# Kernel optimization log

Hardware: AMD Instinct MI355X
Metric: run time of the kernel (lower is better)

Reference implementation:

```python
import jax, jax.numpy as jnp
import numpy as np

B, N, C, H = 64, 4096, 128, 4
ALPHA = 0.2  # leaky_relu negative slope


def setup_inputs() -> dict:
    key = jax.random.key(0)
    k1, k2, k3, k4, k5 = jax.random.split(key, 5)
    V = jax.random.normal(k1, (B, N, C), dtype=jnp.float32)
    graph_size = jax.random.randint(k2, (B,), 1, N + 1, dtype=jnp.int32)
    # xavier_uniform-like init for weight [C, H*C] and tune_weight [1, H, C]
    lim_w = float(np.sqrt(6.0 / (C + H * C)))
    weight = jax.random.uniform(k3, (C, H * C), minval=-lim_w, maxval=lim_w, dtype=jnp.float32)
    lim_t = float(np.sqrt(6.0 / (H + C)))
    tune_weight = jax.random.uniform(k4, (1, H, C), minval=-lim_t, maxval=lim_t, dtype=jnp.float32)
    bias = jnp.full((H * C,), 0.01, dtype=jnp.float32)
    return {"V": V, "graph_size": graph_size, "weight": weight, "bias": bias, "tune_weight": tune_weight}


def reference(V, graph_size, weight, bias, tune_weight):
    # valid-node mask: node n of graph b is valid iff n < graph_size[b]
    mask = jnp.arange(N)[None, :] < graph_size[:, None]          # [B, N]
    # linear projection: [B, N, C] @ [C, H*C] + bias -> [B, N, H, C]
    Vg = (jnp.einsum('bnc,cd->bnd', V, weight) + bias).reshape(B, N, H, C)
    # attention logits per head: sum over features of tune_weight * Vg
    a = jnp.einsum('bnhc,ohc->bnh', Vg, tune_weight)             # [B, N, H]
    a = jnp.where(a >= 0, a, ALPHA * a)                          # leaky_relu
    # per-graph (segment) softmax over valid nodes
    a = jnp.where(mask[:, :, None], a, -jnp.inf)
    a = jax.nn.softmax(a, axis=1)                                # [B, N, H]
    # weighted segment sum -> [B, H, C] -> [B, H*C] (concat=True)
    out = jnp.einsum('bnhc,bnh->bhc', Vg, a)
    return out.reshape(B, H * C)
```

## Files before the change

### kernel.cpp

```cpp
#include <hip/hip_runtime.h>

#define NB 64
#define NN 4096
#define NC 128
#define NH 4
#define HC (NH * NC)
#define PSTRIDE (8 + HC)
#define NSLICE 64
#define TROWS 64
#define LRELU 0.2f

__global__ __launch_bounds__(128) void k0_wt(const float* __restrict__ W,
                                             const float* __restrict__ bias,
                                             const float* __restrict__ tune,
                                             float* __restrict__ wtbt)
{
    const int bid = blockIdx.x;
    const int t = threadIdx.x;
    const float* src = (bid < NC) ? (W + (size_t)bid * HC) : bias;
    float* dst = (bid < NC) ? (wtbt + bid * NH) : (wtbt + NC * NH);
    const float4 a = reinterpret_cast<const float4*>(src)[t];
    const float4 b = reinterpret_cast<const float4*>(tune)[t];
    float p = a.x * b.x + a.y * b.y + a.z * b.z + a.w * b.w;
    #pragma unroll
    for (int off = 16; off; off >>= 1) p += __shfl_xor(p, off, 32);
    if ((t & 31) == 0) dst[t >> 5] = p;
}

__global__ __launch_bounds__(256, 4) void k1_part(const float* __restrict__ V,
                                                  const int* __restrict__ gs,
                                                  const float* __restrict__ wtbt,
                                                  float* __restrict__ part)
{
    __shared__ float smem[8192];
    float (*Vt)[NC] = reinterpret_cast<float(*)[NC]>(smem);
    float (*Sall)[NH][132] = reinterpret_cast<float(*)[NH][132]>(smem);
    float* llds = smem + 8 * NH * 132;

    const int slice = blockIdx.x;
    const int b = blockIdx.y;
    const int tid = threadIdx.x;
    const int hw = tid >> 5;
    const int lane = tid & 31;
    const int h = lane >> 3;
    const int j = lane & 7;
    const int gsz = gs[b];

    const int segB = (gsz + NSLICE - 1) / NSLICE;
    const int myBeg = slice * segB;
    int myEnd = myBeg + segB;
    if (myEnd > gsz) myEnd = gsz;
    const bool hasWork = (myEnd > myBeg);

    float l = 0.f;
    float S[16] = {};

    if (hasWork) {
        float wtk[16];
        #pragma unroll
        for (int u = 0; u < 16; ++u) wtk[u] = wtbt[(16 * j + u) * NH + h];
        const float bt = wtbt[HC + h];

        const float4* Vg4 = reinterpret_cast<const float4*>(V);
        const size_t gbase = (size_t)b * NN;

        float4 r[8];
        #pragma unroll
        for (int k = 0; k < 8; ++k) {
            const int idx = tid + (k << 8);
            const int gr = myBeg + (idx >> 5);
            const int src_row = (gr < myEnd) ? gr : myBeg;
            r[k] = Vg4[(gbase + src_row) * 32 + (idx & 31)];
        }
        #pragma unroll
        for (int k = 0; k < 8; ++k) {
            const int idx = tid + (k << 8);
            reinterpret_cast<float4*>(smem)[idx] = r[k];
        }
        __syncthreads();
        #pragma unroll 2
        for (int rr = 0; rr < 8; ++rr) {
            const int row = (hw << 3) + rr;
            const bool valid = (myBeg + row < myEnd);
            const float4* vr = reinterpret_cast<const float4*>(&Vt[row][j * 16]);
            const float4 A0 = vr[0];
            const float4 A1 = vr[1];
            const float4 A2 = vr[2];
            const float4 A3 = vr[3];
            float a0 = A0.x * wtk[0]  + A0.y * wtk[1]  + A0.z * wtk[2]  + A0.w * wtk[3];
            float a1 = A1.x * wtk[4]  + A1.y * wtk[5]  + A1.z * wtk[6]  + A1.w * wtk[7];
            float a2 = A2.x * wtk[8]  + A2.y * wtk[9]  + A2.z * wtk[10] + A2.w * wtk[11];
            float a3 = A3.x * wtk[12] + A3.y * wtk[13] + A3.z * wtk[14] + A3.w * wtk[15];
            float lg = (a0 + a1) + (a2 + a3);
            lg += __shfl_xor(lg, 1, 32);
            lg += __shfl_xor(lg, 2, 32);
            lg += __shfl_xor(lg, 4, 32);
            float x = lg + bt;
            x = (x >= 0.f) ? x : LRELU * x;
            float p = __expf(x);
            p = valid ? p : 0.f;
            l += p;
            S[0]  += p * A0.x;  S[1]  += p * A0.y;  S[2]  += p * A0.z;  S[3]  += p * A0.w;
            S[4]  += p * A1.x;  S[5]  += p * A1.y;  S[6]  += p * A1.z;  S[7]  += p * A1.w;
            S[8]  += p * A2.x;  S[9]  += p * A2.y;  S[10] += p * A2.z;  S[11] += p * A2.w;
            S[12] += p * A3.x;  S[13] += p * A3.y;  S[14] += p * A3.z;  S[15] += p * A3.w;
        }
        __syncthreads();
    }

    if (j == 0) llds[hw * NH + h] = l;
    #pragma unroll
    for (int t = 0; t < 4; ++t) {
        float4 s4;
        s4.x = S[4 * t]; s4.y = S[4 * t + 1]; s4.z = S[4 * t + 2]; s4.w = S[4 * t + 3];
        *reinterpret_cast<float4*>(&Sall[hw][h][16 * j + 4 * t]) = s4;
    }
    __syncthreads();
    float* pb = part + (size_t)(b * NSLICE + slice) * PSTRIDE;
    if (tid < 4) {
        float L = 0.f;
        #pragma unroll
        for (int ww = 0; ww < 8; ++ww) L += llds[ww * NH + tid];
        pb[4 + tid] = L;
    }
    #pragma unroll
    for (int r2 = 0; r2 < 2; ++r2) {
        const int e = tid + r2 * 256;
        const int hh = e >> 7, k = e & 127;
        float s = 0.f;
        #pragma unroll
        for (int ww = 0; ww < 8; ++ww) s += Sall[ww][hh][k];
        pb[8 + e] = s;
    }
}

__global__ __launch_bounds__(128) void k2_out(const float* __restrict__ part,
                                              const float* __restrict__ W,
                                              const float* __restrict__ bias,
                                              float* __restrict__ out)
{
    const int b = blockIdx.x;
    const int h = blockIdx.y;
    const int tid = threadIdx.x;
    const float* pb = part + (size_t)b * NSLICE * PSTRIDE;

    __shared__ float Sn[NC];
    __shared__ float sL;
    if (tid < 64) {
        float lv = pb[(size_t)tid * PSTRIDE + 4 + h];
        #pragma unroll
        for (int off = 32; off; off >>= 1) lv += __shfl_down(lv, off, 64);
        if (tid == 0) sL = lv;
    }
    __syncthreads();
    {
        float s = 0.f;
        #pragma unroll 8
        for (int c = 0; c < NSLICE; ++c)
            s += pb[(size_t)c * PSTRIDE + 8 + h * NC + tid];
        Sn[tid] = s / sL;
    }
    __syncthreads();
    const int d = h * NC + tid;
    float acc = 0.f;
    #pragma unroll 4
    for (int k = 0; k < NC; ++k) acc += Sn[k] * W[(size_t)k * HC + d];
    out[(size_t)b * HC + d] = acc + bias[d];
}

extern "C" void kernel_launch(void* const* d_in, const int* in_sizes, int n_in,
                              void* d_out, int out_size, void* d_ws, size_t ws_size,
                              hipStream_t stream)
{
    const float* V    = (const float*)d_in[0];
    const int*   gsz  = (const int*)d_in[1];
    const float* W    = (const float*)d_in[2];
    const float* bias = (const float*)d_in[3];
    const float* tune = (const float*)d_in[4];
    float* out  = (float*)d_out;
    float* wtbt = (float*)d_ws;
    float* part = wtbt + PSTRIDE;

    hipLaunchKernelGGL(k0_wt, dim3(NC + 1), dim3(128), 0, stream, W, bias, tune, wtbt);
    hipLaunchKernelGGL(k1_part, dim3(NSLICE, NB), dim3(256), 0, stream, V, gsz, wtbt, part);
    hipLaunchKernelGGL(k2_out, dim3(NB, NH), dim3(128), 0, stream, part, W, bias, out);
}
```

Before: 51.67 us.

## Schedule fixed 64-row tiles across a persistent grid via a precomputed tile table

Per-graph fixed slicing (64 slices per graph regardless of size) is replaced by 64-row tiles. A tile table and per-graph prefix offsets are built in the setup kernel. A persistent grid of 1024 blocks strides over only the tiles that exist, and the output kernel reduces a variable number of partials per graph. The aim is to cut wasted blocks, partially filled row slices and partial-sum traffic for small graphs. In exchange it adds a serial scan in the setup kernel and extra synchronisation per loop iteration.

Measured after the change: 47.30 us. 8.5% less time.

```diff
diff --git a/kernel.cpp b/kernel.cpp
--- a/kernel.cpp
+++ b/kernel.cpp
@@ -6,70 +6,94 @@
 #define NH 4
 #define HC (NH * NC)
 #define PSTRIDE (8 + HC)
-#define NSLICE 64
 #define TROWS 64
+#define NBLK 1024
+#define MAXT 4096
 #define LRELU 0.2f
+
+#define WS_STARTS 520
+#define WS_TABLE  585
+#define WS_PART   (WS_TABLE + MAXT)
 
 __global__ __launch_bounds__(128) void k0_wt(const float* __restrict__ W,
                                              const float* __restrict__ bias,
                                              const float* __restrict__ tune,
-                                             float* __restrict__ wtbt)
+                                             const int* __restrict__ gs,
+                                             float* __restrict__ ws)
 {
     const int bid = blockIdx.x;
     const int t = threadIdx.x;
-    const float* src = (bid < NC) ? (W + (size_t)bid * HC) : bias;
-    float* dst = (bid < NC) ? (wtbt + bid * NH) : (wtbt + NC * NH);
-    const float4 a = reinterpret_cast<const float4*>(src)[t];
-    const float4 b = reinterpret_cast<const float4*>(tune)[t];
-    float p = a.x * b.x + a.y * b.y + a.z * b.z + a.w * b.w;
-    #pragma unroll
-    for (int off = 16; off; off >>= 1) p += __shfl_xor(p, off, 32);
-    if ((t & 31) == 0) dst[t >> 5] = p;
+    if (bid <= NC) {
+        const float* src = (bid < NC) ? (W + (size_t)bid * HC) : bias;
+        float* dst = (bid < NC) ? (ws + bid * NH) : (ws + NC * NH);
+        const float4 a = reinterpret_cast<const float4*>(src)[t];
+        const float4 b = reinterpret_cast<const float4*>(tune)[t];
+        float p = a.x * b.x + a.y * b.y + a.z * b.z + a.w * b.w;
+        #pragma unroll
+        for (int off = 16; off; off >>= 1) p += __shfl_xor(p, off, 32);
+        if ((t & 31) == 0) dst[t >> 5] = p;
+    } else {
+        __shared__ int ntile[NB], st[NB + 1];
+        if (t < NB) ntile[t] = (gs[t] + TROWS - 1) / TROWS;
+        __syncthreads();
+        if (t == 0) {
+            int acc = 0;
+            for (int b2 = 0; b2 < NB; ++b2) { st[b2] = acc; acc += ntile[b2]; }
+            st[NB] = acc;
+        }
+        __syncthreads();
+        int* wsI = reinterpret_cast<int*>(ws);
+        if (t < NB + 1) wsI[WS_STARTS + t] = st[t];
+        if (t < NB) {
+            const int s0 = st[t], n0 = ntile[t];
+            for (int w = 0; w < n0; ++w) wsI[WS_TABLE + s0 + w] = (t << 16) | w;
+        }
+    }
 }
 
 __global__ __launch_bounds__(256, 4) void k1_part(const float* __restrict__ V,
                                                   const int* __restrict__ gs,
-                                                  const float* __restrict__ wtbt,
-                                                  float* __restrict__ part)
+                                                  float* __restrict__ ws)
 {
     __shared__ float smem[8192];
     float (*Vt)[NC] = reinterpret_cast<float(*)[NC]>(smem);
     float (*Sall)[NH][132] = reinterpret_cast<float(*)[NH][132]>(smem);
     float* llds = smem + 8 * NH * 132;
 
-    const int slice = blockIdx.x;
-    const int b = blockIdx.y;
+    const int* wsI = reinterpret_cast<const int*>(ws);
+    const int T = wsI[WS_STARTS + NB];
+    const int* tab = wsI + WS_TABLE;
+    float* part = ws + WS_PART;
+    const float* wtbt = ws;
+
     const int tid = threadIdx.x;
     const int hw = tid >> 5;
     const int lane = tid & 31;
     const int h = lane >> 3;
     const int j = lane & 7;
-    const int gsz = gs[b];
-
-    const int segB = (gsz + NSLICE - 1) / NSLICE;
-    const int myBeg = slice * segB;
-    int myEnd = myBeg + segB;
-    if (myEnd > gsz) myEnd = gsz;
-    const bool hasWork = (myEnd > myBeg);
-
-    float l = 0.f;
-    float S[16] = {};
-
-    if (hasWork) {
-        float wtk[16];
-        #pragma unroll
-        for (int u = 0; u < 16; ++u) wtk[u] = wtbt[(16 * j + u) * NH + h];
-        const float bt = wtbt[HC + h];
-
-        const float4* Vg4 = reinterpret_cast<const float4*>(V);
+
+    float wtk[16];
+    #pragma unroll
+    for (int u = 0; u < 16; ++u) wtk[u] = wtbt[(16 * j + u) * NH + h];
+    const float bt = wtbt[HC + h];
+
+    const float4* Vg4 = reinterpret_cast<const float4*>(V);
+
+    for (int jt = blockIdx.x; jt < T; jt += NBLK) {
+        const int ent = tab[jt];
+        const int b = ent >> 16;
+        const int tbase = (ent & 0xffff) * TROWS;
+        const int gsz = gs[b];
+        int tend = tbase + TROWS;
+        if (tend > gsz) tend = gsz;
         const size_t gbase = (size_t)b * NN;
 
         float4 r[8];
         #pragma unroll
         for (int k = 0; k < 8; ++k) {
             const int idx = tid + (k << 8);
-            const int gr = myBeg + (idx >> 5);
-            const int src_row = (gr < myEnd) ? gr : myBeg;
+            const int gr = tbase + (idx >> 5);
+            const int src_row = (gr < tend) ? gr : tbase;
             r[k] = Vg4[(gbase + src_row) * 32 + (idx & 31)];
         }
         #pragma unroll
@@ -78,10 +102,13 @@
             reinterpret_cast<float4*>(smem)[idx] = r[k];
         }
         __syncthreads();
+
+        float l = 0.f;
+        float S[16] = {};
         #pragma unroll 2
         for (int rr = 0; rr < 8; ++rr) {
             const int row = (hw << 3) + rr;
-            const bool valid = (myBeg + row < myEnd);
+            const bool valid = (tbase + row < tend);
             const float4* vr = reinterpret_cast<const float4*>(&Vt[row][j * 16]);
             const float4 A0 = vr[0];
             const float4 A1 = vr[1];
@@ -106,35 +133,36 @@
             S[12] += p * A3.x;  S[13] += p * A3.y;  S[14] += p * A3.z;  S[15] += p * A3.w;
         }
         __syncthreads();
-    }
-
-    if (j == 0) llds[hw * NH + h] = l;
-    #pragma unroll
-    for (int t = 0; t < 4; ++t) {
-        float4 s4;
-        s4.x = S[4 * t]; s4.y = S[4 * t + 1]; s4.z = S[4 * t + 2]; s4.w = S[4 * t + 3];
-        *reinterpret_cast<float4*>(&Sall[hw][h][16 * j + 4 * t]) = s4;
-    }
-    __syncthreads();
-    float* pb = part + (size_t)(b * NSLICE + slice) * PSTRIDE;
-    if (tid < 4) {
-        float L = 0.f;
-        #pragma unroll
-        for (int ww = 0; ww < 8; ++ww) L += llds[ww * NH + tid];
-        pb[4 + tid] = L;
-    }
-    #pragma unroll
-    for (int r2 = 0; r2 < 2; ++r2) {
-        const int e = tid + r2 * 256;
-        const int hh = e >> 7, k = e & 127;
-        float s = 0.f;
-        #pragma unroll
-        for (int ww = 0; ww < 8; ++ww) s += Sall[ww][hh][k];
-        pb[8 + e] = s;
-    }
-}
-
-__global__ __launch_bounds__(128) void k2_out(const float* __restrict__ part,
+
+        if (j == 0) llds[hw * NH + h] = l;
+        #pragma unroll
+        for (int t2 = 0; t2 < 4; ++t2) {
+            float4 s4;
+            s4.x = S[4 * t2]; s4.y = S[4 * t2 + 1]; s4.z = S[4 * t2 + 2]; s4.w = S[4 * t2 + 3];
+            *reinterpret_cast<float4*>(&Sall[hw][h][16 * j + 4 * t2]) = s4;
+        }
+        __syncthreads();
+        float* pb = part + (size_t)jt * PSTRIDE;
+        if (tid < 4) {
+            float L = 0.f;
+            #pragma unroll
+            for (int ww = 0; ww < 8; ++ww) L += llds[ww * NH + tid];
+            pb[4 + tid] = L;
+        }
+        #pragma unroll
+        for (int r2 = 0; r2 < 2; ++r2) {
+            const int e = tid + r2 * 256;
+            const int hh = e >> 7, k = e & 127;
+            float s = 0.f;
+            #pragma unroll
+            for (int ww = 0; ww < 8; ++ww) s += Sall[ww][hh][k];
+            pb[8 + e] = s;
+        }
+        __syncthreads();
+    }
+}
+
+__global__ __launch_bounds__(128) void k2_out(const float* __restrict__ ws,
                                               const float* __restrict__ W,
                                               const float* __restrict__ bias,
                                               float* __restrict__ out)
@@ -142,12 +170,15 @@
     const int b = blockIdx.x;
     const int h = blockIdx.y;
     const int tid = threadIdx.x;
-    const float* pb = part + (size_t)b * NSLICE * PSTRIDE;
+    const int* wsI = reinterpret_cast<const int*>(ws);
+    const int s0 = wsI[WS_STARTS + b];
+    const int n0 = wsI[WS_STARTS + b + 1] - s0;
+    const float* pb = ws + WS_PART + (size_t)s0 * PSTRIDE;
 
     __shared__ float Sn[NC];
     __shared__ float sL;
     if (tid < 64) {
-        float lv = pb[(size_t)tid * PSTRIDE + 4 + h];
+        float lv = (tid < n0) ? pb[(size_t)tid * PSTRIDE + 4 + h] : 0.f;
         #pragma unroll
         for (int off = 32; off; off >>= 1) lv += __shfl_down(lv, off, 64);
         if (tid == 0) sL = lv;
@@ -155,8 +186,7 @@
     __syncthreads();
     {
         float s = 0.f;
-        #pragma unroll 8
-        for (int c = 0; c < NSLICE; ++c)
+        for (int c = 0; c < n0; ++c)
             s += pb[(size_t)c * PSTRIDE + 8 + h * NC + tid];
         Sn[tid] = s / sL;
     }
@@ -177,11 +207,10 @@
     const float* W    = (const float*)d_in[2];
     const float* bias = (const float*)d_in[3];
     const float* tune = (const float*)d_in[4];
-    float* out  = (float*)d_out;
-    float* wtbt = (float*)d_ws;
-    float* part = wtbt + PSTRIDE;
-
-    hipLaunchKernelGGL(k0_wt, dim3(NC + 1), dim3(128), 0, stream, W, bias, tune, wtbt);
-    hipLaunchKernelGGL(k1_part, dim3(NSLICE, NB), dim3(256), 0, stream, V, gsz, wtbt, part);
-    hipLaunchKernelGGL(k2_out, dim3(NB, NH), dim3(128), 0, stream, part, W, bias, out);
-}
+    float* out = (float*)d_out;
+    float* ws  = (float*)d_ws;
+
+    hipLaunchKernelGGL(k0_wt, dim3(NC + 2), dim3(128), 0, stream, W, bias, tune, gsz, ws);
+    hipLaunchKernelGGL(k1_part, dim3(NBLK), dim3(256), 0, stream, V, gsz, ws);
+    hipLaunchKernelGGL(k2_out, dim3(NB, NH), dim3(128), 0, stream, ws, W, bias, out);
+}
```
